# Optimization experiments

Measured on AMD Instinct MI355X. Metric: run time of the kernel, lower is better.

## Reference

```python
import jax, jax.numpy as jnp
import numpy as np
import math

B, T, C, H = 2, 2048, 512, 8
TOPK = 64
HD = C // H
EPS = 1e-12  # torch F.normalize eps


def setup_inputs() -> dict:
    key = jax.random.key(0)
    ks = jax.random.split(key, 6)
    s = 1.0 / math.sqrt(C)
    q = jax.random.normal(ks[0], (B, T, C), dtype=jnp.float32)
    tgt_mask = jnp.tril(jnp.ones((T, T), dtype=jnp.float32)).reshape(1, 1, T, T)
    Wq = jax.random.normal(ks[1], (C, C), dtype=jnp.float32) * s
    Wk = jax.random.normal(ks[2], (C, C), dtype=jnp.float32) * s
    Wv = jax.random.normal(ks[3], (C, C), dtype=jnp.float32) * s
    Wp = jax.random.normal(ks[4], (C, C), dtype=jnp.float32) * s
    bq = jnp.zeros((C,), jnp.float32)
    bk = jnp.zeros((C,), jnp.float32)
    bv = jnp.zeros((C,), jnp.float32)
    bp = jnp.zeros((C,), jnp.float32)
    return {"q": q, "tgt_mask": tgt_mask, "Wq": Wq, "bq": bq, "Wk": Wk, "bk": bk,
            "Wv": Wv, "bv": bv, "Wp": Wp, "bp": bp}


def _attn(q, tgt_mask, Wq, bq, Wk, bk, Wv, bv, Wp, bp):
    Bt, Tt, Ct = q.shape
    # self-attention: k = v = q (module path when k, v are None)
    qh = (q @ Wq + bq).reshape(Bt, Tt, H, HD).transpose(0, 2, 1, 3)  # [B,H,T,hd]
    kh = (q @ Wk + bk).reshape(Bt, Tt, H, HD).transpose(0, 2, 1, 3)
    vh = (q @ Wv + bv).reshape(Bt, Tt, H, HD).transpose(0, 2, 1, 3)
    # L2-normalize v along head dim (F.normalize, p=2, eps=1e-12)
    vn = jnp.linalg.norm(vh, axis=-1, keepdims=True)
    vh = vh / jnp.maximum(vn, EPS)
    att = jnp.einsum('bhqd,bhkd->bhqk', qh, kh) * (1.0 / math.sqrt(HD))
    neg = -jnp.inf
    att = jnp.where(tgt_mask[:, :, :Tt, :Tt] == 0, neg, att)
    # top-k sparsification: drop entries strictly below the k-th largest per row
    top = jax.lax.top_k(att, TOPK)[0]            # [B,H,T,TOPK]
    vk = top[..., -1:]                            # k-th largest threshold
    att = jnp.where(att < vk, neg, att)
    att = jax.nn.softmax(att, axis=-1)
    y = jnp.einsum('bhqk,bhkd->bhqd', att, vh)
    y = y.transpose(0, 2, 1, 3).reshape(Bt, Tt, Ct)
    return y @ Wp + bp


def reference(q, tgt_mask, Wq, bq, Wk, bk, Wv, bv, Wp, bp):
    return _attn(q, tgt_mask, Wq, bq, Wk, bk, Wv, bv, Wp, bp)
```

## Files before the change

kernel.cpp:

```cpp
#include <hip/hip_runtime.h>
#include <cstdint>
#include <math.h>

static constexpr int Bc = 2, Tc = 2048, Cch = 512, Hc = 8;
static constexpr int BT = Bc * Tc;
static constexpr int NBH = Bc * Hc;
static constexpr int NRT = Tc / 128;
static constexpr int NTRI = NRT * (NRT + 1) / 2;
static constexpr size_t TRI_FLOATS = (size_t)NTRI * 16384;

typedef float f32x4 __attribute__((ext_vector_type(4)));
typedef short s16x8 __attribute__((ext_vector_type(8)));
typedef unsigned short u16x8 __attribute__((ext_vector_type(8)));
typedef unsigned short u16x4 __attribute__((ext_vector_type(4)));

__device__ __host__ inline constexpr int tri_i(int r) { return r * (r + 1) / 2; }

__device__ inline float wave_sum_f(float x) {
#pragma unroll
  for (int o = 32; o; o >>= 1) x += __shfl_xor(x, o);
  return x;
}
__device__ inline unsigned short f2bf(float x) {
  unsigned u = __float_as_uint(x);
  return (unsigned short)((u + 0x7FFFu + ((u >> 16) & 1u)) >> 16);
}
__device__ inline float bf2f(unsigned short h) { return __uint_as_float(((unsigned)h) << 16); }
__device__ inline float su2f(unsigned s) {
  unsigned u = (s & 0x80000000u) ? (s ^ 0x80000000u) : ~s;
  return __uint_as_float(u);
}

__global__ __launch_bounds__(256) void split_k(const float* __restrict__ X,
    unsigned short* __restrict__ hi, unsigned short* __restrict__ lo, int n8) {
  int i = blockIdx.x * 256 + threadIdx.x;
  if (i >= n8) return;
  const f32x4* p = (const f32x4*)X + (size_t)i * 2;
  f32x4 a = p[0], b = p[1];
  float v[8] = {a[0], a[1], a[2], a[3], b[0], b[1], b[2], b[3]};
  u16x8 h, l;
#pragma unroll
  for (int c = 0; c < 8; c++) {
    unsigned short hh = f2bf(v[c]);
    h[c] = hh;
    l[c] = f2bf(v[c] - bf2f(hh));
  }
  *(u16x8*)(hi + (size_t)i * 8) = h;
  *(u16x8*)(lo + (size_t)i * 8) = l;
}

__global__ __launch_bounds__(256) void splitT4_k(const float* __restrict__ Wq,
    const float* __restrict__ Wk, const float* __restrict__ Wv,
    const float* __restrict__ Wp, unsigned short* __restrict__ wsp) {
  const int z = blockIdx.z;
  const float* W = (z == 0) ? Wq : (z == 1) ? Wk : (z == 2) ? Wv : Wp;
  unsigned short* hiT = wsp + (size_t)z * 524288;
  unsigned short* loT = hiT + 262144;
  __shared__ float t[64][65];
  const int tid = threadIdx.x;
  const int k0 = blockIdx.x * 64, n0 = blockIdx.y * 64;
#pragma unroll
  for (int p = 0; p < 4; p++) {
    int idx = tid + p * 256, kk = idx >> 4, n4 = idx & 15;
    f32x4 v = *(const f32x4*)&W[(size_t)(k0 + kk) * Cch + n0 + n4 * 4];
    t[kk][n4 * 4 + 0] = v[0]; t[kk][n4 * 4 + 1] = v[1];
    t[kk][n4 * 4 + 2] = v[2]; t[kk][n4 * 4 + 3] = v[3];
  }
  __syncthreads();
  {
    int n = tid >> 2, ks = tid & 3;
    u16x8 h0, h1, l0, l1;
#pragma unroll
    for (int kk = 0; kk < 8; kk++) {
      float x = t[ks * 16 + kk][n];
      unsigned short hh = f2bf(x);
      h0[kk] = hh; l0[kk] = f2bf(x - bf2f(hh));
      float y = t[ks * 16 + 8 + kk][n];
      unsigned short hy = f2bf(y);
      h1[kk] = hy; l1[kk] = f2bf(y - bf2f(hy));
    }
    size_t base = (size_t)(n0 + n) * Cch + k0 + ks * 16;
    *(u16x8*)(hiT + base) = h0; *(u16x8*)(hiT + base + 8) = h1;
    *(u16x8*)(loT + base) = l0; *(u16x8*)(loT + base + 8) = l1;
  }
}

template <int BF16OUT>
__global__ __launch_bounds__(256) void gemm3_k(
    const unsigned short* __restrict__ Ahi, const unsigned short* __restrict__ Alo,
    const unsigned short* __restrict__ Bhi, const unsigned short* __restrict__ Blo,
    const float* __restrict__ bias, void* __restrict__ Out) {
  __shared__ unsigned short Ah[2][64][72];
  __shared__ unsigned short Bs[2][64][72];
  const int tid = threadIdx.x;
  const int w = tid >> 6, lane = tid & 63, e = lane >> 4, lr = lane & 15;
  const int wr = w >> 1, wc = w & 1;
  const int brow = blockIdx.y * 64, bcol = blockIdx.x * 64;
  f32x4 acc[2][2] = {};
  for (int k0 = 0; k0 < Cch; k0 += 64) {
#pragma unroll
    for (int p = 0; p < 2; p++) {
      int idx = tid + p * 256, row = idx >> 3, seg = idx & 7;
      *(u16x8*)&Ah[0][row][seg * 8] = *(const u16x8*)&Ahi[(size_t)(brow + row) * Cch + k0 + seg * 8];
      *(u16x8*)&Ah[1][row][seg * 8] = *(const u16x8*)&Alo[(size_t)(brow + row) * Cch + k0 + seg * 8];
      *(u16x8*)&Bs[0][row][seg * 8] = *(const u16x8*)&Bhi[(size_t)(bcol + row) * Cch + k0 + seg * 8];
      *(u16x8*)&Bs[1][row][seg * 8] = *(const u16x8*)&Blo[(size_t)(bcol + row) * Cch + k0 + seg * 8];
    }
    __syncthreads();
#pragma unroll
    for (int ks = 0; ks < 2; ks++) {
      s16x8 ah[2], al[2], bh[2], bl[2];
#pragma unroll
      for (int ti = 0; ti < 2; ti++) {
        ah[ti] = *(const s16x8*)&Ah[0][wr * 32 + ti * 16 + lr][ks * 32 + e * 8];
        al[ti] = *(const s16x8*)&Ah[1][wr * 32 + ti * 16 + lr][ks * 32 + e * 8];
      }
#pragma unroll
      for (int tj = 0; tj < 2; tj++) {
        bh[tj] = *(const s16x8*)&Bs[0][wc * 32 + tj * 16 + lr][ks * 32 + e * 8];
        bl[tj] = *(const s16x8*)&Bs[1][wc * 32 + tj * 16 + lr][ks * 32 + e * 8];
      }
#pragma unroll
      for (int ti = 0; ti < 2; ti++)
#pragma unroll
        for (int tj = 0; tj < 2; tj++) {
          acc[ti][tj] = __builtin_amdgcn_mfma_f32_16x16x32_bf16(ah[ti], bh[tj], acc[ti][tj], 0, 0, 0);
          acc[ti][tj] = __builtin_amdgcn_mfma_f32_16x16x32_bf16(ah[ti], bl[tj], acc[ti][tj], 0, 0, 0);
          acc[ti][tj] = __builtin_amdgcn_mfma_f32_16x16x32_bf16(al[ti], bh[tj], acc[ti][tj], 0, 0, 0);
        }
    }
    __syncthreads();
  }
#pragma unroll
  for (int ti = 0; ti < 2; ti++)
#pragma unroll
    for (int tj = 0; tj < 2; tj++) {
      int col = bcol + wc * 32 + tj * 16 + lr;
      float bi = bias[col];
#pragma unroll
      for (int r = 0; r < 4; r++) {
        int row = brow + wr * 32 + ti * 16 + e * 4 + r;
        float v = acc[ti][tj][r] + bi;
        if (BF16OUT) ((unsigned short*)Out)[(size_t)row * Cch + col] = f2bf(v);
        else         ((float*)Out)[(size_t)row * Cch + col] = v;
      }
    }
}

__global__ __launch_bounds__(256) void gemm3_qkv_k(
    const unsigned short* __restrict__ Ahi, const unsigned short* __restrict__ Alo,
    const unsigned short* __restrict__ wsp,
    const float* __restrict__ bq, const float* __restrict__ bk, const float* __restrict__ bv,
    unsigned short* __restrict__ Qp, unsigned short* __restrict__ Kp, float* __restrict__ Vf) {
  const int z = blockIdx.z;
  const unsigned short* Bhi = wsp + (size_t)z * 524288;
  const unsigned short* Blo = Bhi + 262144;
  const float* bias = (z == 0) ? bq : (z == 1) ? bk : bv;
  __shared__ unsigned short Ah[2][64][72];
  __shared__ unsigned short Bs[2][64][72];
  const int tid = threadIdx.x;
  const int w = tid >> 6, lane = tid & 63, e = lane >> 4, lr = lane & 15;
  const int wr = w >> 1, wc = w & 1;
  const int brow = blockIdx.y * 64, bcol = blockIdx.x * 64;
  f32x4 acc[2][2] = {};
  for (int k0 = 0; k0 < Cch; k0 += 64) {
#pragma unroll
    for (int p = 0; p < 2; p++) {
      int idx = tid + p * 256, row = idx >> 3, seg = idx & 7;
      *(u16x8*)&Ah[0][row][seg * 8] = *(const u16x8*)&Ahi[(size_t)(brow + row) * Cch + k0 + seg * 8];
      *(u16x8*)&Ah[1][row][seg * 8] = *(const u16x8*)&Alo[(size_t)(brow + row) * Cch + k0 + seg * 8];
      *(u16x8*)&Bs[0][row][seg * 8] = *(const u16x8*)&Bhi[(size_t)(bcol + row) * Cch + k0 + seg * 8];
      *(u16x8*)&Bs[1][row][seg * 8] = *(const u16x8*)&Blo[(size_t)(bcol + row) * Cch + k0 + seg * 8];
    }
    __syncthreads();
#pragma unroll
    for (int ks = 0; ks < 2; ks++) {
      s16x8 ah[2], al[2], bh[2], bl[2];
#pragma unroll
      for (int ti = 0; ti < 2; ti++) {
        ah[ti] = *(const s16x8*)&Ah[0][wr * 32 + ti * 16 + lr][ks * 32 + e * 8];
        al[ti] = *(const s16x8*)&Ah[1][wr * 32 + ti * 16 + lr][ks * 32 + e * 8];
      }
#pragma unroll
      for (int tj = 0; tj < 2; tj++) {
        bh[tj] = *(const s16x8*)&Bs[0][wc * 32 + tj * 16 + lr][ks * 32 + e * 8];
        bl[tj] = *(const s16x8*)&Bs[1][wc * 32 + tj * 16 + lr][ks * 32 + e * 8];
      }
#pragma unroll
      for (int ti = 0; ti < 2; ti++)
#pragma unroll
        for (int tj = 0; tj < 2; tj++) {
          acc[ti][tj] = __builtin_amdgcn_mfma_f32_16x16x32_bf16(ah[ti], bh[tj], acc[ti][tj], 0, 0, 0);
          acc[ti][tj] = __builtin_amdgcn_mfma_f32_16x16x32_bf16(ah[ti], bl[tj], acc[ti][tj], 0, 0, 0);
          acc[ti][tj] = __builtin_amdgcn_mfma_f32_16x16x32_bf16(al[ti], bh[tj], acc[ti][tj], 0, 0, 0);
        }
    }
    __syncthreads();
  }
#pragma unroll
  for (int ti = 0; ti < 2; ti++)
#pragma unroll
    for (int tj = 0; tj < 2; tj++) {
      int col = bcol + wc * 32 + tj * 16 + lr;
      float bi = bias[col];
#pragma unroll
      for (int r = 0; r < 4; r++) {
        int row = brow + wr * 32 + ti * 16 + e * 4 + r;
        float v = acc[ti][tj][r] + bi;
        size_t g = (size_t)row * Cch + col;
        if (z == 0) Qp[g] = f2bf(v);
        else if (z == 1) Kp[g] = f2bf(v);
        else Vf[g] = v;
      }
    }
}

__global__ __launch_bounds__(256) void vnormt_k(const float* __restrict__ Vf,
                                                unsigned short* __restrict__ Vt) {
  __shared__ unsigned short T[64][72];
  const int tid = threadIdx.x;
  const int t0 = blockIdx.x * 64;
  const int h = blockIdx.y;
  const int tok = tid >> 2;
  const int q = tid & 3;
  const float* src = Vf + (size_t)(t0 + tok) * Cch + h * 64 + q * 16;
  f32x4 v[4];
  float ss = 0.f;
#pragma unroll
  for (int i = 0; i < 4; i++) {
    v[i] = *(const f32x4*)(src + i * 4);
#pragma unroll
    for (int c = 0; c < 4; c++) ss += v[i][c] * v[i][c];
  }
  ss += __shfl_xor(ss, 1);
  ss += __shfl_xor(ss, 2);
  float inv = 1.0f / fmaxf(sqrtf(ss), 1e-12f);
#pragma unroll
  for (int i = 0; i < 4; i++)
#pragma unroll
    for (int c = 0; c < 4; c++)
      T[q * 16 + i * 4 + c][tok] = f2bf(v[i][c] * inv);
  __syncthreads();
  const int d = tid >> 2, s2 = (tid & 3) * 2;
  const int b = t0 >> 11;
  size_t base = ((size_t)((b * Hc + h) * 64 + d)) * Tc + (t0 & 2047);
  *(u16x8*)(Vt + base + s2 * 8)     = *(const u16x8*)&T[d][s2 * 8];
  *(u16x8*)(Vt + base + s2 * 8 + 8) = *(const u16x8*)&T[d][s2 * 8 + 8];
}

__global__ __launch_bounds__(512) void sqk_k(const unsigned short* __restrict__ Qp,
    const unsigned short* __restrict__ Kp, float* __restrict__ S, int bh0) {
  __shared__ unsigned short Qs[128][72], Ks[128][72];
  int rt, ct;
  {
    int i = blockIdx.x;
    int r = (int)((sqrtf(8.f * i + 1.f) - 1.f) * 0.5f);
    while ((r + 1) * (r + 2) / 2 <= i) r++;
    while (r * (r + 1) / 2 > i) r--;
    rt = r; ct = i - r * (r + 1) / 2;
  }
  const int bh = bh0 + blockIdx.y, b = bh >> 3, h = bh & 7;
  const int tid = threadIdx.x, w = tid >> 6, lane = tid & 63, e = lane >> 4, lr = lane & 15;
#pragma unroll
  for (int p = 0; p < 2; p++) {
    int idx = tid + p * 512, row = idx >> 3, seg = idx & 7;
    *(u16x8*)&Qs[row][seg * 8] = *(const u16x8*)&Qp[((size_t)(b * Tc + rt * 128 + row)) * Cch + h * 64 + seg * 8];
    *(u16x8*)&Ks[row][seg * 8] = *(const u16x8*)&Kp[((size_t)(b * Tc + ct * 128 + row)) * Cch + h * 64 + seg * 8];
  }
  __syncthreads();
  f32x4 acc[8] = {};
  s16x8 a[2];
#pragma unroll
  for (int ks = 0; ks < 2; ks++) a[ks] = *(const s16x8*)&Qs[w * 16 + lr][ks * 32 + e * 8];
#pragma unroll
  for (int tj = 0; tj < 8; tj++) {
#pragma unroll
    for (int ks = 0; ks < 2; ks++) {
      s16x8 bb = *(const s16x8*)&Ks[tj * 16 + lr][ks * 32 + e * 8];
      acc[tj] = __builtin_amdgcn_mfma_f32_16x16x32_bf16(a[ks], bb, acc[tj], 0, 0, 0);
    }
  }
  float* Srow0 = S + (size_t)(bh - bh0) * TRI_FLOATS + (size_t)tri_i(rt) * 16384;
  const int stride = (rt + 1) * 128;
#pragma unroll
  for (int tj = 0; tj < 8; tj++)
#pragma unroll
    for (int r = 0; r < 4; r++) {
      int row = w * 16 + e * 4 + r;
      Srow0[(size_t)row * stride + ct * 128 + tj * 16 + lr] = acc[tj][r] * 0.125f;
    }
}

__global__ __launch_bounds__(512, 4) void sel_k(float* __restrict__ S) {
  int bidr = (int)gridDim.x - 1 - (int)blockIdx.x;
  int wid = bidr * 8 + (threadIdx.x >> 6);
  int lane = threadIdx.x & 63;
  int bhl = wid >> 11, t = wid & 2047;
  int rt = t >> 7, lrow = t & 127;
  int stride = (rt + 1) * 128;
  float* row = S + (size_t)bhl * TRI_FLOATS + (size_t)tri_i(rt) * 16384 + (size_t)lrow * stride;
  unsigned su[32];
#pragma unroll
  for (int c = 0; c < 8; c++) {
    if (c * 256 < stride) {
      int j0 = c * 256 + lane * 4;
      f32x4 v;
      if (j0 < stride) v = *(const f32x4*)(row + j0);
      else { v[0] = v[1] = v[2] = v[3] = -INFINITY; }
#pragma unroll
      for (int cc = 0; cc < 4; cc++) {
        float x = (j0 + cc <= t) ? v[cc] : -INFINITY;
        unsigned u = __float_as_uint(x);
        su[c * 4 + cc] = (u & 0x80000000u) ? ~u : (u | 0x80000000u);
      }
    } else {
#pragma unroll
      for (int cc = 0; cc < 4; cc++) su[c * 4 + cc] = 0x007FFFFFu;
    }
  }
  unsigned lo = 0;
#pragma unroll 1
  for (int bit = 31; bit >= 0; bit--) {
    unsigned cand = lo | (1u << bit);
    int cnt = 0;
#pragma unroll
    for (int c = 0; c < 8; c++)
      if (c * 256 < stride)
#pragma unroll
        for (int q = 0; q < 4; q++)
          cnt += (int)__popcll(__ballot(su[c * 4 + q] >= cand));
    if (cnt >= 64) {
      lo = cand;
      if (cnt == 64) {
        unsigned mn = 0xFFFFFFFFu;
#pragma unroll
        for (int c = 0; c < 8; c++)
          if (c * 256 < stride)
#pragma unroll
            for (int q = 0; q < 4; q++) { unsigned x = (su[c * 4 + q] >= cand) ? su[c * 4 + q] : 0xFFFFFFFFu; mn = mn < x ? mn : x; }
#pragma unroll
        for (int o = 32; o; o >>= 1) { unsigned x = (unsigned)__shfl_xor((int)mn, o); mn = mn < x ? mn : x; }
        lo = mn;
        break;
      }
    }
  }
  unsigned mx = 0;
#pragma unroll
  for (int c = 0; c < 8; c++)
    if (c * 256 < stride)
#pragma unroll
      for (int q = 0; q < 4; q++) mx = mx > su[c * 4 + q] ? mx : su[c * 4 + q];
#pragma unroll
  for (int o = 32; o; o >>= 1) { unsigned x = (unsigned)__shfl_xor((int)mx, o); mx = mx > x ? mx : x; }
  float m = su2f(mx);
  float sum = 0.f;
#pragma unroll
  for (int c = 0; c < 8; c++)
    if (c * 256 < stride)
#pragma unroll
      for (int q = 0; q < 4; q++) {
        float v = su2f(su[c * 4 + q]);
        float wv = (su[c * 4 + q] >= lo) ? __expf(v - m) : 0.f;
        su[c * 4 + q] = __float_as_uint(wv);
        sum += wv;
      }
  sum = wave_sum_f(sum);
  float inv = 1.f / sum;
  unsigned short* prow = (unsigned short*)row;
#pragma unroll
  for (int c = 0; c < 8; c++) {
    if (c * 256 < stride) {
      int j0 = c * 256 + lane * 4;
      if (j0 < stride) {
        u16x4 pk;
#pragma unroll
        for (int cc = 0; cc < 4; cc++) pk[cc] = f2bf(__uint_as_float(su[c * 4 + cc]) * inv);
        *(u16x4*)(prow + j0) = pk;
      }
    }
  }
}

__global__ __launch_bounds__(512) void pv_k(const float* __restrict__ S,
    const unsigned short* __restrict__ Vt,
    unsigned short* __restrict__ Yhi, unsigned short* __restrict__ Ylo, int bh0) {
  __shared__ unsigned short Ps[128][136];
  __shared__ unsigned short Vs[64][136];
  const int rt = (int)gridDim.x - 1 - (int)blockIdx.x;
  const int bh = bh0 + blockIdx.y, b = bh >> 3, h = bh & 7;
  const int tid = threadIdx.x, w = tid >> 6, lane = tid & 63, e = lane >> 4, lr = lane & 15;
  const int stride = (rt + 1) * 128;
  const float* Srow0 = S + (size_t)(bh - bh0) * TRI_FLOATS + (size_t)tri_i(rt) * 16384;
  f32x4 acc[4] = {};
  for (int kt = 0; kt <= rt; kt++) {
#pragma unroll
    for (int p = 0; p < 4; p++) {
      int idx = tid + p * 512, row = idx >> 4, seg = idx & 15;
      const unsigned short* src = (const unsigned short*)(Srow0 + (size_t)row * stride) + kt * 128 + seg * 8;
      *(u16x8*)&Ps[row][seg * 8] = *(const u16x8*)src;
    }
#pragma unroll
    for (int p = 0; p < 2; p++) {
      int idx = tid + p * 512, d = idx >> 4, seg = idx & 15;
      *(u16x8*)&Vs[d][seg * 8] = *(const u16x8*)&Vt[((size_t)(bh * 64 + d)) * Tc + kt * 128 + seg * 8];
    }
    __syncthreads();
#pragma unroll
    for (int ks = 0; ks < 4; ks++) {
      s16x8 a = *(const s16x8*)&Ps[w * 16 + lr][ks * 32 + e * 8];
#pragma unroll
      for (int tj = 0; tj < 4; tj++) {
        s16x8 bb = *(const s16x8*)&Vs[tj * 16 + lr][ks * 32 + e * 8];
        acc[tj] = __builtin_amdgcn_mfma_f32_16x16x32_bf16(a, bb, acc[tj], 0, 0, 0);
      }
    }
    __syncthreads();
  }
#pragma unroll
  for (int tj = 0; tj < 4; tj++)
#pragma unroll
    for (int r = 0; r < 4; r++) {
      int row = rt * 128 + w * 16 + e * 4 + r;
      size_t g = ((size_t)(b * Tc + row)) * Cch + h * 64 + tj * 16 + lr;
      float y = acc[tj][r];
      unsigned short hh = f2bf(y);
      Yhi[g] = hh;
      Ylo[g] = f2bf(y - bf2f(hh));
    }
}

extern "C" void kernel_launch(void* const* d_in, const int* in_sizes, int n_in,
                              void* d_out, int out_size, void* d_ws, size_t ws_size,
                              hipStream_t stream) {
  const float* q  = (const float*)d_in[0];
  const float* Wq = (const float*)d_in[2];
  const float* bq = (const float*)d_in[3];
  const float* Wk = (const float*)d_in[4];
  const float* bk = (const float*)d_in[5];
  const float* Wv = (const float*)d_in[6];
  const float* bv = (const float*)d_in[7];
  const float* Wp = (const float*)d_in[8];
  const float* bp = (const float*)d_in[9];
  float* out = (float*)d_out;
  char* ws = (char*)d_ws;
  constexpr size_t MB = 1u << 20;

  unsigned short* qhi = (unsigned short*)(ws + 0 * MB);
  unsigned short* qlo = (unsigned short*)(ws + 4 * MB);
  unsigned short* Qp  = (unsigned short*)(ws + 8 * MB);
  unsigned short* Kp  = (unsigned short*)(ws + 12 * MB);
  unsigned short* Vt  = (unsigned short*)(ws + 16 * MB);
  unsigned short* wsp = (unsigned short*)(ws + 20 * MB);
  float* Sb = (float*)(ws + 24 * MB);
  float* Vf = (float*)(ws + 24 * MB);
  unsigned short* Yhi = qhi;
  unsigned short* Ylo = qlo;

  int nbh = NBH;
  while (nbh > 1 && 24 * MB + TRI_FLOATS * 4 * (size_t)nbh > ws_size) nbh >>= 1;

  split_k<<<(BT * Cch / 8 + 255) / 256, 256, 0, stream>>>(q, qhi, qlo, BT * Cch / 8);
  splitT4_k<<<dim3(8, 8, 4), 256, 0, stream>>>(Wq, Wk, Wv, Wp, wsp);

  gemm3_qkv_k<<<dim3(Cch / 64, BT / 64, 3), 256, 0, stream>>>(
      qhi, qlo, wsp, bq, bk, bv, Qp, Kp, Vf);
  vnormt_k<<<dim3(BT / 64, Hc), 256, 0, stream>>>(Vf, Vt);

  for (int c = 0; c < NBH / nbh; c++) {
    int bh0 = c * nbh;
    sqk_k<<<dim3(NTRI, nbh), 512, 0, stream>>>(Qp, Kp, Sb, bh0);
    sel_k<<<nbh * 256, 512, 0, stream>>>(Sb);
    pv_k<<<dim3(NRT, nbh), 512, 0, stream>>>(Sb, Vt, Yhi, Ylo, bh0);
  }

  gemm3_k<0><<<dim3(Cch / 64, BT / 64), 256, 0, stream>>>(
      Yhi, qlo , wsp + (size_t)6 * 262144, wsp + (size_t)7 * 262144, bp, out);
}
```

Measured before the change: 209.4 us.

## Process two rows per wave in top-k select and split PV blocks by row halves

The selection kernel now has each wave handle two adjacent rows, interleaving their radix bit-search ballots to add independent work per wave and halving the grid. The PV kernel splits each 128-row tile into two 64-row halves, each with its own block, and assigns each wave a 16-row by 32-dim output slice, doubling the grid for better occupancy and load balance on the triangular workload. The cost is twice the registers in the select kernel, which may reduce occupancy. In PV, each V tile is now loaded twice, once by each half-block.

```diff
diff --git a/kernel.cpp b/kernel.cpp
--- a/kernel.cpp
+++ b/kernel.cpp
@@ -292,91 +292,138 @@
 }
 
 __global__ __launch_bounds__(512, 4) void sel_k(float* __restrict__ S) {
-  int bidr = (int)gridDim.x - 1 - (int)blockIdx.x;
-  int wid = bidr * 8 + (threadIdx.x >> 6);
-  int lane = threadIdx.x & 63;
-  int bhl = wid >> 11, t = wid & 2047;
-  int rt = t >> 7, lrow = t & 127;
-  int stride = (rt + 1) * 128;
-  float* row = S + (size_t)bhl * TRI_FLOATS + (size_t)tri_i(rt) * 16384 + (size_t)lrow * stride;
-  unsigned su[32];
+  const int bidr = (int)gridDim.x - 1 - (int)blockIdx.x;
+  const int w = threadIdx.x >> 6, lane = threadIdx.x & 63;
+  const int wid = bidr * 16 + w * 2;
+  const int bhl = wid >> 11, t0 = wid & 2047;
+  const int rt = t0 >> 7, lrow = t0 & 127;
+  const int stride = (rt + 1) * 128;
+  float* row0 = S + (size_t)bhl * TRI_FLOATS + (size_t)tri_i(rt) * 16384 + (size_t)lrow * stride;
+  float* row1 = row0 + stride;
+  const int t1 = t0 + 1;
+
+  unsigned su0[32], su1[32];
 #pragma unroll
   for (int c = 0; c < 8; c++) {
     if (c * 256 < stride) {
       int j0 = c * 256 + lane * 4;
-      f32x4 v;
-      if (j0 < stride) v = *(const f32x4*)(row + j0);
-      else { v[0] = v[1] = v[2] = v[3] = -INFINITY; }
+      f32x4 v0, v1;
+      if (j0 < stride) { v0 = *(const f32x4*)(row0 + j0); v1 = *(const f32x4*)(row1 + j0); }
+      else { v0[0]=v0[1]=v0[2]=v0[3]=-INFINITY; v1=v0; }
 #pragma unroll
       for (int cc = 0; cc < 4; cc++) {
-        float x = (j0 + cc <= t) ? v[cc] : -INFINITY;
-        unsigned u = __float_as_uint(x);
-        su[c * 4 + cc] = (u & 0x80000000u) ? ~u : (u | 0x80000000u);
+        float x0 = (j0 + cc <= t0) ? v0[cc] : -INFINITY;
+        unsigned u0 = __float_as_uint(x0);
+        su0[c * 4 + cc] = (u0 & 0x80000000u) ? ~u0 : (u0 | 0x80000000u);
+        float x1 = (j0 + cc <= t1) ? v1[cc] : -INFINITY;
+        unsigned u1 = __float_as_uint(x1);
+        su1[c * 4 + cc] = (u1 & 0x80000000u) ? ~u1 : (u1 | 0x80000000u);
       }
     } else {
 #pragma unroll
-      for (int cc = 0; cc < 4; cc++) su[c * 4 + cc] = 0x007FFFFFu;
-    }
-  }
-  unsigned lo = 0;
+      for (int cc = 0; cc < 4; cc++) { su0[c * 4 + cc] = 0x007FFFFFu; su1[c * 4 + cc] = 0x007FFFFFu; }
+    }
+  }
+  unsigned lo0 = 0, lo1 = 0;
+  bool done0 = false, done1 = false;
 #pragma unroll 1
   for (int bit = 31; bit >= 0; bit--) {
-    unsigned cand = lo | (1u << bit);
-    int cnt = 0;
-#pragma unroll
-    for (int c = 0; c < 8; c++)
-      if (c * 256 < stride)
-#pragma unroll
-        for (int q = 0; q < 4; q++)
-          cnt += (int)__popcll(__ballot(su[c * 4 + q] >= cand));
-    if (cnt >= 64) {
-      lo = cand;
-      if (cnt == 64) {
-        unsigned mn = 0xFFFFFFFFu;
-#pragma unroll
-        for (int c = 0; c < 8; c++)
-          if (c * 256 < stride)
-#pragma unroll
-            for (int q = 0; q < 4; q++) { unsigned x = (su[c * 4 + q] >= cand) ? su[c * 4 + q] : 0xFFFFFFFFu; mn = mn < x ? mn : x; }
-#pragma unroll
-        for (int o = 32; o; o >>= 1) { unsigned x = (unsigned)__shfl_xor((int)mn, o); mn = mn < x ? mn : x; }
-        lo = mn;
-        break;
-      }
-    }
-  }
-  unsigned mx = 0;
+    if (done0 && done1) break;
+    unsigned bmask = 1u << bit;
+    if (!done0) {
+      unsigned cand = lo0 | bmask;
+      int cnt = 0;
+#pragma unroll
+      for (int c = 0; c < 8; c++)
+        if (c * 256 < stride)
+#pragma unroll
+          for (int q = 0; q < 4; q++)
+            cnt += (int)__popcll(__ballot(su0[c * 4 + q] >= cand));
+      if (cnt >= 64) {
+        lo0 = cand;
+        if (cnt == 64) {
+          unsigned mn = 0xFFFFFFFFu;
+#pragma unroll
+          for (int c = 0; c < 8; c++)
+            if (c * 256 < stride)
+#pragma unroll
+              for (int q = 0; q < 4; q++) { unsigned x = (su0[c * 4 + q] >= cand) ? su0[c * 4 + q] : 0xFFFFFFFFu; mn = mn < x ? mn : x; }
+#pragma unroll
+          for (int o = 32; o; o >>= 1) { unsigned x = (unsigned)__shfl_xor((int)mn, o); mn = mn < x ? mn : x; }
+          lo0 = mn; done0 = true;
+        }
+      }
+    }
+    if (!done1) {
+      unsigned cand = lo1 | bmask;
+      int cnt = 0;
+#pragma unroll
+      for (int c = 0; c < 8; c++)
+        if (c * 256 < stride)
+#pragma unroll
+          for (int q = 0; q < 4; q++)
+            cnt += (int)__popcll(__ballot(su1[c * 4 + q] >= cand));
+      if (cnt >= 64) {
+        lo1 = cand;
+        if (cnt == 64) {
+          unsigned mn = 0xFFFFFFFFu;
+#pragma unroll
+          for (int c = 0; c < 8; c++)
+            if (c * 256 < stride)
+#pragma unroll
+              for (int q = 0; q < 4; q++) { unsigned x = (su1[c * 4 + q] >= cand) ? su1[c * 4 + q] : 0xFFFFFFFFu; mn = mn < x ? mn : x; }
+#pragma unroll
+          for (int o = 32; o; o >>= 1) { unsigned x = (unsigned)__shfl_xor((int)mn, o); mn = mn < x ? mn : x; }
+          lo1 = mn; done1 = true;
+        }
+      }
+    }
+  }
+  unsigned mx0 = 0, mx1 = 0;
 #pragma unroll
   for (int c = 0; c < 8; c++)
     if (c * 256 < stride)
 #pragma unroll
-      for (int q = 0; q < 4; q++) mx = mx > su[c * 4 + q] ? mx : su[c * 4 + q];
-#pragma unroll
-  for (int o = 32; o; o >>= 1) { unsigned x = (unsigned)__shfl_xor((int)mx, o); mx = mx > x ? mx : x; }
-  float m = su2f(mx);
-  float sum = 0.f;
+      for (int q = 0; q < 4; q++) {
+        mx0 = mx0 > su0[c * 4 + q] ? mx0 : su0[c * 4 + q];
+        mx1 = mx1 > su1[c * 4 + q] ? mx1 : su1[c * 4 + q];
+      }
+#pragma unroll
+  for (int o = 32; o; o >>= 1) {
+    unsigned x0 = (unsigned)__shfl_xor((int)mx0, o); mx0 = mx0 > x0 ? mx0 : x0;
+    unsigned x1 = (unsigned)__shfl_xor((int)mx1, o); mx1 = mx1 > x1 ? mx1 : x1;
+  }
+  float m0 = su2f(mx0), m1 = su2f(mx1);
+  float sum0 = 0.f, sum1 = 0.f;
 #pragma unroll
   for (int c = 0; c < 8; c++)
     if (c * 256 < stride)
 #pragma unroll
       for (int q = 0; q < 4; q++) {
-        float v = su2f(su[c * 4 + q]);
-        float wv = (su[c * 4 + q] >= lo) ? __expf(v - m) : 0.f;
-        su[c * 4 + q] = __float_as_uint(wv);
-        sum += wv;
-      }
-  sum = wave_sum_f(sum);
-  float inv = 1.f / sum;
-  unsigned short* prow = (unsigned short*)row;
+        float v0 = su2f(su0[c * 4 + q]);
+        float w0 = (su0[c * 4 + q] >= lo0) ? __expf(v0 - m0) : 0.f;
+        su0[c * 4 + q] = __float_as_uint(w0); sum0 += w0;
+        float v1 = su2f(su1[c * 4 + q]);
+        float w1 = (su1[c * 4 + q] >= lo1) ? __expf(v1 - m1) : 0.f;
+        su1[c * 4 + q] = __float_as_uint(w1); sum1 += w1;
+      }
+  sum0 = wave_sum_f(sum0); sum1 = wave_sum_f(sum1);
+  float inv0 = 1.f / sum0, inv1 = 1.f / sum1;
+  unsigned short* p0 = (unsigned short*)row0;
+  unsigned short* p1 = (unsigned short*)row1;
 #pragma unroll
   for (int c = 0; c < 8; c++) {
     if (c * 256 < stride) {
       int j0 = c * 256 + lane * 4;
       if (j0 < stride) {
-        u16x4 pk;
-#pragma unroll
-        for (int cc = 0; cc < 4; cc++) pk[cc] = f2bf(__uint_as_float(su[c * 4 + cc]) * inv);
-        *(u16x4*)(prow + j0) = pk;
+        u16x4 pk0, pk1;
+#pragma unroll
+        for (int cc = 0; cc < 4; cc++) {
+          pk0[cc] = f2bf(__uint_as_float(su0[c * 4 + cc]) * inv0);
+          pk1[cc] = f2bf(__uint_as_float(su1[c * 4 + cc]) * inv1);
+        }
+        *(u16x4*)(p0 + j0) = pk0;
+        *(u16x4*)(p1 + j0) = pk1;
       }
     }
   }
@@ -385,44 +432,45 @@
 __global__ __launch_bounds__(512) void pv_k(const float* __restrict__ S,
     const unsigned short* __restrict__ Vt,
     unsigned short* __restrict__ Yhi, unsigned short* __restrict__ Ylo, int bh0) {
-  __shared__ unsigned short Ps[128][136];
+  __shared__ unsigned short Ps[64][136];
   __shared__ unsigned short Vs[64][136];
-  const int rt = (int)gridDim.x - 1 - (int)blockIdx.x;
+  const int x = blockIdx.x;
+  const int rt = NRT - 1 - (x >> 1);
+  const int half = x & 1;
   const int bh = bh0 + blockIdx.y, b = bh >> 3, h = bh & 7;
   const int tid = threadIdx.x, w = tid >> 6, lane = tid & 63, e = lane >> 4, lr = lane & 15;
   const int stride = (rt + 1) * 128;
+  const int rbase = half * 64;
   const float* Srow0 = S + (size_t)(bh - bh0) * TRI_FLOATS + (size_t)tri_i(rt) * 16384;
-  f32x4 acc[4] = {};
+  const int rg = w & 3, dh = w >> 2;
+  f32x4 acc[2] = {};
   for (int kt = 0; kt <= rt; kt++) {
 #pragma unroll
-    for (int p = 0; p < 4; p++) {
-      int idx = tid + p * 512, row = idx >> 4, seg = idx & 15;
-      const unsigned short* src = (const unsigned short*)(Srow0 + (size_t)row * stride) + kt * 128 + seg * 8;
-      *(u16x8*)&Ps[row][seg * 8] = *(const u16x8*)src;
-    }
-#pragma unroll
     for (int p = 0; p < 2; p++) {
-      int idx = tid + p * 512, d = idx >> 4, seg = idx & 15;
-      *(u16x8*)&Vs[d][seg * 8] = *(const u16x8*)&Vt[((size_t)(bh * 64 + d)) * Tc + kt * 128 + seg * 8];
+      int idx = tid + p * 512, pr = idx >> 4, seg = idx & 15;
+      const unsigned short* src =
+          (const unsigned short*)(Srow0 + (size_t)(rbase + pr) * stride) + kt * 128 + seg * 8;
+      *(u16x8*)&Ps[pr][seg * 8] = *(const u16x8*)src;
+      *(u16x8*)&Vs[pr][seg * 8] = *(const u16x8*)&Vt[((size_t)(bh * 64 + pr)) * Tc + kt * 128 + seg * 8];
     }
     __syncthreads();
 #pragma unroll
     for (int ks = 0; ks < 4; ks++) {
-      s16x8 a = *(const s16x8*)&Ps[w * 16 + lr][ks * 32 + e * 8];
-#pragma unroll
-      for (int tj = 0; tj < 4; tj++) {
-        s16x8 bb = *(const s16x8*)&Vs[tj * 16 + lr][ks * 32 + e * 8];
+      s16x8 a = *(const s16x8*)&Ps[rg * 16 + lr][ks * 32 + e * 8];
+#pragma unroll
+      for (int tj = 0; tj < 2; tj++) {
+        s16x8 bb = *(const s16x8*)&Vs[dh * 32 + tj * 16 + lr][ks * 32 + e * 8];
         acc[tj] = __builtin_amdgcn_mfma_f32_16x16x32_bf16(a, bb, acc[tj], 0, 0, 0);
       }
     }
     __syncthreads();
   }
 #pragma unroll
-  for (int tj = 0; tj < 4; tj++)
+  for (int tj = 0; tj < 2; tj++)
 #pragma unroll
     for (int r = 0; r < 4; r++) {
-      int row = rt * 128 + w * 16 + e * 4 + r;
-      size_t g = ((size_t)(b * Tc + row)) * Cch + h * 64 + tj * 16 + lr;
+      int row = rt * 128 + rbase + rg * 16 + e * 4 + r;
+      size_t g = ((size_t)(b * Tc + row)) * Cch + h * 64 + dh * 32 + tj * 16 + lr;
       float y = acc[tj][r];
       unsigned short hh = f2bf(y);
       Yhi[g] = hh;
@@ -470,8 +518,8 @@
   for (int c = 0; c < NBH / nbh; c++) {
     int bh0 = c * nbh;
     sqk_k<<<dim3(NTRI, nbh), 512, 0, stream>>>(Qp, Kp, Sb, bh0);
-    sel_k<<<nbh * 256, 512, 0, stream>>>(Sb);
-    pv_k<<<dim3(NRT, nbh), 512, 0, stream>>>(Sb, Vt, Yhi, Ylo, bh0);
+    sel_k<<<nbh * 128, 512, 0, stream>>>(Sb);
+    pv_k<<<dim3(2 * NRT, nbh), 512, 0, stream>>>(Sb, Vt, Yhi, Ylo, bh0);
   }
 
   gemm3_k<0><<<dim3(Cch / 64, BT / 64), 256, 0, stream>>>(
```

Result: slower. 234.2 us (+11.8%).
